# Kernel optimization log

Measured on AMD Instinct MI355X. Metric: run time of the kernel, lower is better.

## Reference

```python
import jax, jax.numpy as jnp
import numpy as np

N_NODES = 100000
N_EDGES = 3200000
N_FEAT = 512
N_GRAPHS = 64
N_EXTRA_LAYERS = 3  # layers 2..4, all 1->1


def setup_inputs() -> dict:
    key = jax.random.key(0)
    ks = jax.random.split(key, 10)
    x = jax.random.normal(ks[0], (N_NODES, N_FEAT), dtype=jnp.float32)
    edge_src = jax.random.randint(ks[1], (N_EDGES,), 0, N_NODES, dtype=jnp.int32)
    edge_dst = jax.random.randint(ks[2], (N_EDGES,), 0, N_NODES, dtype=jnp.int32)
    graph_ids = jnp.sort(jax.random.randint(ks[3], (N_NODES,), 0, N_GRAPHS, dtype=jnp.int32))
    W_neigh0 = jax.random.normal(ks[4], (N_FEAT, 1), dtype=jnp.float32) * 0.05
    W_self0 = jax.random.normal(ks[5], (N_FEAT, 1), dtype=jnp.float32) * 0.05
    b0 = jax.random.normal(ks[6], (1,), dtype=jnp.float32)
    W_neigh_r = jax.random.normal(ks[7], (N_EXTRA_LAYERS, 1, 1), dtype=jnp.float32)
    W_self_r = jax.random.normal(ks[8], (N_EXTRA_LAYERS, 1, 1), dtype=jnp.float32)
    b_r = jax.random.normal(ks[9], (N_EXTRA_LAYERS, 1), dtype=jnp.float32)
    return {"x": x, "edge_src": edge_src, "edge_dst": edge_dst, "graph_ids": graph_ids,
            "W_neigh0": W_neigh0, "W_self0": W_self0, "b0": b0,
            "W_neigh_r": W_neigh_r, "W_self_r": W_self_r, "b_r": b_r}


def _conv_wl(h, edge_src, edge_dst, W_neigh, W_self, b, n_nodes):
    # GraphConv(norm='none'): project first (in >= out here), gather at src, scatter-sum at dst, + bias
    proj = h @ W_neigh                      # [N, out]
    neigh = jax.ops.segment_sum(proj[edge_src], edge_dst, num_segments=n_nodes) + b
    return neigh + h @ W_self               # residual self-loop linear (no bias)


def reference(x, edge_src, edge_dst, graph_ids, W_neigh0, W_self0, b0, W_neigh_r, W_self_r, b_r):
    n = x.shape[0]
    xs = [x]
    h = jax.nn.relu(_conv_wl(x, edge_src, edge_dst, W_neigh0, W_self0, b0, n))
    xs.append(h)
    for i in range(W_neigh_r.shape[0]):
        h = jax.nn.relu(_conv_wl(h, edge_src, edge_dst, W_neigh_r[i], W_self_r[i], b_r[i], n))
        xs.append(h)
    hcat = jnp.concatenate(xs, axis=1)       # [N, F + num_layers] (concat_features=True)
    # dgl.sum_nodes: per-graph sum over the batched graph
    return jax.ops.segment_sum(hcat, graph_ids, num_segments=N_GRAPHS)  # [G, F + L]
```

## Files before the change

kernel.cpp:

```cpp
#include <hip/hip_runtime.h>

#define N_NODES  100000
#define N_EDGES  3200000
#define N_FEAT   512
#define N_GRAPHS 64
#define N_COLS   516
#define NBINS    1563
#define B1       256
#define EPB      (N_EDGES / B1)
#define CHUNK    25
#define NWAVES   (N_NODES / CHUNK)
#define SRC_MASK 0x1FFFF

__global__ __launch_bounds__(1024) void prep_kernel(
    const int* __restrict__ edst, const int* __restrict__ gid,
    int* __restrict__ histG, int* __restrict__ starts, float* __restrict__ outz)
{
    __shared__ int lh[NBINS];
    const int b = blockIdx.x, tid = threadIdx.x;
    const int gtid = b * 1024 + tid;

    if (gtid < N_GRAPHS * N_COLS) outz[gtid] = 0.f;
    if (gtid < N_NODES) {
        const int g = gid[gtid];
        const int gp = gtid ? gid[gtid - 1] : -1;
        for (int q = gp + 1; q <= g; ++q) starts[q] = gtid;
        if (gtid == N_NODES - 1)
            for (int q = g + 1; q <= N_GRAPHS; ++q) starts[q] = N_NODES;
    }
    for (int i = tid; i < NBINS; i += 1024) lh[i] = 0;
    __syncthreads();
    const int e0 = b * EPB;
    for (int e = e0 + tid; e < e0 + EPB; e += 1024)
        atomicAdd(&lh[edst[e] >> 6], 1);
    __syncthreads();
    for (int i = tid; i < NBINS; i += 1024) histG[i * B1 + b] = lh[i];
}

__device__ __forceinline__ void flush_cs(
    int si, int cur_g, const float a[8], int wave, int lane,
    float* __restrict__ pp, int* __restrict__ pt, float* __restrict__ out)
{
    if (si < 2) {
        const int slot = wave * 2 + si;
        if (lane == 0) pt[slot] = cur_g;
        float* d = pp + (size_t)slot * N_FEAT + lane * 8;
        *(float4*)d       = make_float4(a[0], a[1], a[2], a[3]);
        *(float4*)(d + 4) = make_float4(a[4], a[5], a[6], a[7]);
    } else {
        float* o = out + (size_t)cur_g * N_COLS + lane * 8;
        #pragma unroll
        for (int k = 0; k < 8; ++k) atomicAdd(o + k, a[k]);
    }
}

__global__ __launch_bounds__(256) void pass_x_kernel(
    const float* __restrict__ x, const int* __restrict__ gid,
    const float* __restrict__ wn, const float* __restrict__ ws,
    float* __restrict__ p0, float* __restrict__ s0,
    float* __restrict__ neigh, float* __restrict__ out,
    float* __restrict__ pp, int* __restrict__ pt)
{
    const int wave = (blockIdx.x * blockDim.x + threadIdx.x) >> 6;
    const int lane = threadIdx.x & 63;
    const int start = wave * CHUNK, end = start + CHUNK;

    for (int n = start + lane; n < end; n += 64) neigh[n] = 0.f;

    const float4 wna = *(const float4*)(wn + lane * 8);
    const float4 wnb = *(const float4*)(wn + lane * 8 + 4);
    const float4 wsa = *(const float4*)(ws + lane * 8);
    const float4 wsb = *(const float4*)(ws + lane * 8 + 4);

    float a[8] = {0.f, 0.f, 0.f, 0.f, 0.f, 0.f, 0.f, 0.f};
    int cur_g = gid[start];
    const bool uniform = (gid[end - 1] == cur_g);
    int si = 0;

    for (int n = start; n < end; ++n) {
        if (!uniform) {
            const int g = gid[n];
            if (g != cur_g) {
                flush_cs(si, cur_g, a, wave, lane, pp, pt, out);
                ++si;
                #pragma unroll
                for (int k = 0; k < 8; ++k) a[k] = 0.f;
                cur_g = g;
            }
        }
        const float* row = x + (size_t)n * N_FEAT;
        const float4 xa = *(const float4*)(row + lane * 8);
        const float4 xb = *(const float4*)(row + lane * 8 + 4);

        a[0] += xa.x; a[1] += xa.y; a[2] += xa.z; a[3] += xa.w;
        a[4] += xb.x; a[5] += xb.y; a[6] += xb.z; a[7] += xb.w;

        float dn = xa.x*wna.x + xa.y*wna.y + xa.z*wna.z + xa.w*wna.w
                 + xb.x*wnb.x + xb.y*wnb.y + xb.z*wnb.z + xb.w*wnb.w;
        float dv = xa.x*wsa.x + xa.y*wsa.y + xa.z*wsa.z + xa.w*wsa.w
                 + xb.x*wsb.x + xb.y*wsb.y + xb.z*wsb.z + xb.w*wsb.w;
        #pragma unroll
        for (int off = 32; off > 0; off >>= 1) {
            dn += __shfl_down(dn, off);
            dv += __shfl_down(dv, off);
        }
        if (lane == 0) { p0[n] = dn; s0[n] = dv; }
    }
    flush_cs(si, cur_g, a, wave, lane, pp, pt, out);
    ++si;
    if (lane == 0)
        for (int s2 = si; s2 < 2; ++s2) pt[wave * 2 + s2] = -1;
}

__global__ __launch_bounds__(512) void reduce_x_kernel(
    const float* __restrict__ pp, const int* __restrict__ pt,
    const int* __restrict__ starts, float* __restrict__ out)
{
    const int g = blockIdx.x, c = threadIdx.x;
    const int s = starts[g], e = starts[g + 1];
    float acc = 0.f;
    if (e > s) {
        const int w0 = s / CHUNK, w1 = (e - 1) / CHUNK;
        for (int w = w0; w <= w1; ++w) {
            #pragma unroll
            for (int k = 0; k < 2; ++k) {
                const int slot = w * 2 + k;
                if (pt[slot] == g) acc += pp[(size_t)slot * N_FEAT + c];
            }
        }
    }
    out[(size_t)g * N_COLS + c] += acc;
}

__global__ __launch_bounds__(256) void colscan_kernel(
    const int* __restrict__ histG, int* __restrict__ colscanG,
    int* __restrict__ totalG)
{
    __shared__ int sc[256];
    const int bin = blockIdx.x, t = threadIdx.x;
    const int v = histG[bin * B1 + t];
    sc[t] = v;
    __syncthreads();
    for (int off = 1; off < 256; off <<= 1) {
        const int a = (t >= off) ? sc[t - off] : 0;
        __syncthreads();
        sc[t] += a;
        __syncthreads();
    }
    colscanG[bin * B1 + t] = sc[t] - v;
    if (t == 255) totalG[bin] = sc[255];
}

__global__ __launch_bounds__(256) void scan2_kernel(
    const int* __restrict__ totalG, int* __restrict__ binstart)
{
    __shared__ int sc[256];
    const int t = threadIdx.x;
    const int CH = 7;
    int loc[CH];
    int s = 0;
    for (int i = 0; i < CH; ++i) {
        const int bin = t * CH + i;
        const int v = (bin < NBINS) ? totalG[bin] : 0;
        loc[i] = s; s += v;
    }
    const int my = s;
    sc[t] = my;
    __syncthreads();
    for (int off = 1; off < 256; off <<= 1) {
        const int a = (t >= off) ? sc[t - off] : 0;
        __syncthreads();
        sc[t] += a;
        __syncthreads();
    }
    const int texcl = sc[t] - my;
    for (int i = 0; i < CH; ++i) {
        const int bin = t * CH + i;
        if (bin < NBINS) binstart[bin] = texcl + loc[i];
    }
    if (t == 255) binstart[NBINS] = sc[255];
}

__global__ __launch_bounds__(1024) void reorder_kernel(
    const int* __restrict__ esrc, const int* __restrict__ edst,
    const int* __restrict__ binstart, const int* __restrict__ colscanG,
    int* __restrict__ sorted)
{
    __shared__ int offs[NBINS];
    const int b = blockIdx.x, tid = threadIdx.x;
    for (int i = tid; i < NBINS; i += 1024)
        offs[i] = binstart[i] + colscanG[i * B1 + b];
    __syncthreads();
    const int e0 = b * EPB;
    for (int e = e0 + tid; e < e0 + EPB; e += 1024) {
        const int s = esrc[e], d = edst[e];
        const int p = atomicAdd(&offs[d >> 6], 1);
        sorted[p] = s | ((d & 63) << 17);
    }
}

__global__ __launch_bounds__(256) void binned_scatter_kernel(
    const int* __restrict__ sorted, const int* __restrict__ binstart,
    const float* __restrict__ pin, const float* __restrict__ self_in,
    const float* __restrict__ wself_p, const float* __restrict__ bias_p,
    const float* __restrict__ wnext_p,
    float* __restrict__ h_out, float* __restrict__ p_next,
    const int* __restrict__ gid, float* __restrict__ out, int col)
{
    __shared__ float acc[4][64];
    const int b = blockIdx.x, tid = threadIdx.x;
    ((float*)acc)[tid] = 0.f;
    __syncthreads();

    const int st = binstart[b], en = binstart[b + 1];
    const int w = tid >> 6;
    for (int e = st + tid; e < en; e += 256) {
        const int v = sorted[e];
        atomicAdd(&acc[w][v >> 17], pin[v & SRC_MASK]);
    }
    __syncthreads();

    if (tid < 64) {
        const int n = b * 64 + tid;
        const bool valid = (n < N_NODES);
        float h = 0.f;
        int g = 0;
        if (valid) {
            const float nb = acc[0][tid] + acc[1][tid] + acc[2][tid] + acc[3][tid];
            const float sw = wself_p ? *wself_p : 1.0f;
            const float v = nb + *bias_p + sw * self_in[n];
            h = v > 0.f ? v : 0.f;
            h_out[n] = h;
            if (wnext_p) p_next[n] = h * (*wnext_p);
            g = gid[n];
        }
        const int g0 = __shfl(g, 0);
        if (__all(!valid || g == g0)) {
            float s = h;
            #pragma unroll
            for (int off = 32; off > 0; off >>= 1) s += __shfl_down(s, off);
            if (tid == 0) atomicAdd(&out[(size_t)g0 * N_COLS + col], s);
        } else if (valid) {
            atomicAdd(&out[(size_t)g * N_COLS + col], h);
        }
    }
}

extern "C" void kernel_launch(void* const* d_in, const int* in_sizes, int n_in,
                              void* d_out, int out_size, void* d_ws, size_t ws_size,
                              hipStream_t stream)
{
    (void)in_sizes; (void)n_in; (void)out_size; (void)ws_size;

    const float* x    = (const float*)d_in[0];
    const int*   esrc = (const int*)d_in[1];
    const int*   edst = (const int*)d_in[2];
    const int*   gid  = (const int*)d_in[3];
    const float* Wn0  = (const float*)d_in[4];
    const float* Ws0  = (const float*)d_in[5];
    const float* b0p  = (const float*)d_in[6];
    const float* Wnr  = (const float*)d_in[7];
    const float* Wsr  = (const float*)d_in[8];
    const float* brp  = (const float*)d_in[9];
    float* out = (float*)d_out;

    float* pp    = (float*)d_ws;
    float* bufP  = pp + (size_t)NWAVES * 2 * N_FEAT;
    float* bufP2 = bufP  + N_NODES;
    float* bufS  = bufP2 + N_NODES;
    float* bufH  = bufS  + N_NODES;
    int*   pt       = (int*)(bufH + N_NODES);
    int*   starts   = pt + NWAVES * 2;
    int*   binstart = starts + (N_GRAPHS + 1);
    int*   totalG   = binstart + NBINS + 1;
    int*   histG    = totalG + NBINS;
    int*   colscanG = histG + (size_t)NBINS * B1;
    int*   sorted   = colscanG + (size_t)NBINS * B1;

    prep_kernel<<<B1, 1024, 0, stream>>>(edst, gid, histG, starts, out);
    pass_x_kernel<<<NWAVES / 4, 256, 0, stream>>>(
        x, gid, Wn0, Ws0, bufP, bufS, bufP2 ,
        out, pp, pt);
    colscan_kernel<<<NBINS, 256, 0, stream>>>(histG, colscanG, totalG);
    scan2_kernel<<<1, 256, 0, stream>>>(totalG, binstart);
    reorder_kernel<<<B1, 1024, 0, stream>>>(esrc, edst, binstart, colscanG, sorted);
    reduce_x_kernel<<<N_GRAPHS, 512, 0, stream>>>(pp, pt, starts, out);

    binned_scatter_kernel<<<NBINS, 256, 0, stream>>>(
        sorted, binstart, bufP, bufS, nullptr, b0p, Wnr + 0, bufH, bufP2, gid, out, 512);
    binned_scatter_kernel<<<NBINS, 256, 0, stream>>>(
        sorted, binstart, bufP2, bufH, Wsr + 0, brp + 0, Wnr + 1, bufH, bufP, gid, out, 513);
    binned_scatter_kernel<<<NBINS, 256, 0, stream>>>(
        sorted, binstart, bufP, bufH, Wsr + 1, brp + 1, Wnr + 2, bufH, bufP2, gid, out, 514);
    binned_scatter_kernel<<<NBINS, 256, 0, stream>>>(
        sorted, binstart, bufP2, bufH, Wsr + 2, brp + 2, nullptr, bufH, nullptr, gid, out, 515);
}
```

Measured before the change: 508.5 us.

## Fuse scan stages via last-block pattern and merge reorder with graph reduce

Merges the column scan and the global bin scan into one kernel, where the last block to finish (detected with an atomic counter) computes the bin starts. The per-graph reduce is folded into the reorder launch as extra blocks. The x pass now uses nontemporal loads, drops the unused zeroing of the neigh buffer, and uses a smaller node chunk per wave. Together these remove two kernel launches and their tail gaps. The cost is a serialized tail in the last scan block and more partial-sum slots to reduce.

```diff
diff --git a/kernel.cpp b/kernel.cpp
--- a/kernel.cpp
+++ b/kernel.cpp
@@ -8,18 +8,22 @@
 #define NBINS    1563
 #define B1       256
 #define EPB      (N_EDGES / B1)
-#define CHUNK    25
+#define CHUNK    20
 #define NWAVES   (N_NODES / CHUNK)
 #define SRC_MASK 0x1FFFF
 
+typedef float f4v __attribute__((ext_vector_type(4)));
+
 __global__ __launch_bounds__(1024) void prep_kernel(
     const int* __restrict__ edst, const int* __restrict__ gid,
-    int* __restrict__ histG, int* __restrict__ starts, float* __restrict__ outz)
+    int* __restrict__ histG, int* __restrict__ starts,
+    float* __restrict__ outz, int* __restrict__ done)
 {
     __shared__ int lh[NBINS];
     const int b = blockIdx.x, tid = threadIdx.x;
     const int gtid = b * 1024 + tid;
 
+    if (gtid == 0) *done = 0;
     if (gtid < N_GRAPHS * N_COLS) outz[gtid] = 0.f;
     if (gtid < N_NODES) {
         const int g = gid[gtid];
@@ -58,14 +62,11 @@
     const float* __restrict__ x, const int* __restrict__ gid,
     const float* __restrict__ wn, const float* __restrict__ ws,
     float* __restrict__ p0, float* __restrict__ s0,
-    float* __restrict__ neigh, float* __restrict__ out,
-    float* __restrict__ pp, int* __restrict__ pt)
+    float* __restrict__ out, float* __restrict__ pp, int* __restrict__ pt)
 {
     const int wave = (blockIdx.x * blockDim.x + threadIdx.x) >> 6;
     const int lane = threadIdx.x & 63;
     const int start = wave * CHUNK, end = start + CHUNK;
-
-    for (int n = start + lane; n < end; n += 64) neigh[n] = 0.f;
 
     const float4 wna = *(const float4*)(wn + lane * 8);
     const float4 wnb = *(const float4*)(wn + lane * 8 + 4);
@@ -89,8 +90,8 @@
             }
         }
         const float* row = x + (size_t)n * N_FEAT;
-        const float4 xa = *(const float4*)(row + lane * 8);
-        const float4 xb = *(const float4*)(row + lane * 8 + 4);
+        const f4v xa = __builtin_nontemporal_load((const f4v*)(row + lane * 8));
+        const f4v xb = __builtin_nontemporal_load((const f4v*)(row + lane * 8 + 4));
 
         a[0] += xa.x; a[1] += xa.y; a[2] += xa.z; a[3] += xa.w;
         a[4] += xb.x; a[5] += xb.y; a[6] += xb.z; a[7] += xb.w;
@@ -112,31 +113,12 @@
         for (int s2 = si; s2 < 2; ++s2) pt[wave * 2 + s2] = -1;
 }
 
-__global__ __launch_bounds__(512) void reduce_x_kernel(
-    const float* __restrict__ pp, const int* __restrict__ pt,
-    const int* __restrict__ starts, float* __restrict__ out)
-{
-    const int g = blockIdx.x, c = threadIdx.x;
-    const int s = starts[g], e = starts[g + 1];
-    float acc = 0.f;
-    if (e > s) {
-        const int w0 = s / CHUNK, w1 = (e - 1) / CHUNK;
-        for (int w = w0; w <= w1; ++w) {
-            #pragma unroll
-            for (int k = 0; k < 2; ++k) {
-                const int slot = w * 2 + k;
-                if (pt[slot] == g) acc += pp[(size_t)slot * N_FEAT + c];
-            }
-        }
-    }
-    out[(size_t)g * N_COLS + c] += acc;
-}
-
-__global__ __launch_bounds__(256) void colscan_kernel(
+__global__ __launch_bounds__(256) void scan_fused_kernel(
     const int* __restrict__ histG, int* __restrict__ colscanG,
-    int* __restrict__ totalG)
+    int* __restrict__ totalG, int* __restrict__ binstart, int* __restrict__ done)
 {
     __shared__ int sc[256];
+    __shared__ int lastflag;
     const int bin = blockIdx.x, t = threadIdx.x;
     const int v = histG[bin * B1 + t];
     sc[t] = v;
@@ -149,22 +131,23 @@
     }
     colscanG[bin * B1 + t] = sc[t] - v;
     if (t == 255) totalG[bin] = sc[255];
-}
-
-__global__ __launch_bounds__(256) void scan2_kernel(
-    const int* __restrict__ totalG, int* __restrict__ binstart)
-{
-    __shared__ int sc[256];
-    const int t = threadIdx.x;
+
+    __threadfence();
+    if (t == 0) lastflag = (atomicAdd(done, 1) == NBINS - 1);
+    __syncthreads();
+    if (!lastflag) return;
+    __threadfence();
+
     const int CH = 7;
     int loc[CH];
     int s = 0;
     for (int i = 0; i < CH; ++i) {
-        const int bin = t * CH + i;
-        const int v = (bin < NBINS) ? totalG[bin] : 0;
-        loc[i] = s; s += v;
+        const int b2 = t * CH + i;
+        const int vv = (b2 < NBINS) ? totalG[b2] : 0;
+        loc[i] = s; s += vv;
     }
     const int my = s;
+    __syncthreads();
     sc[t] = my;
     __syncthreads();
     for (int off = 1; off < 256; off <<= 1) {
@@ -175,27 +158,47 @@
     }
     const int texcl = sc[t] - my;
     for (int i = 0; i < CH; ++i) {
-        const int bin = t * CH + i;
-        if (bin < NBINS) binstart[bin] = texcl + loc[i];
+        const int b2 = t * CH + i;
+        if (b2 < NBINS) binstart[b2] = texcl + loc[i];
     }
     if (t == 255) binstart[NBINS] = sc[255];
 }
 
-__global__ __launch_bounds__(1024) void reorder_kernel(
+__global__ __launch_bounds__(1024) void reorder_reduce_kernel(
     const int* __restrict__ esrc, const int* __restrict__ edst,
     const int* __restrict__ binstart, const int* __restrict__ colscanG,
-    int* __restrict__ sorted)
-{
-    __shared__ int offs[NBINS];
+    int* __restrict__ sorted,
+    const float* __restrict__ pp, const int* __restrict__ pt,
+    const int* __restrict__ starts, float* __restrict__ out)
+{
     const int b = blockIdx.x, tid = threadIdx.x;
-    for (int i = tid; i < NBINS; i += 1024)
-        offs[i] = binstart[i] + colscanG[i * B1 + b];
-    __syncthreads();
-    const int e0 = b * EPB;
-    for (int e = e0 + tid; e < e0 + EPB; e += 1024) {
-        const int s = esrc[e], d = edst[e];
-        const int p = atomicAdd(&offs[d >> 6], 1);
-        sorted[p] = s | ((d & 63) << 17);
+    if (b < B1) {
+        __shared__ int offs[NBINS];
+        for (int i = tid; i < NBINS; i += 1024)
+            offs[i] = binstart[i] + colscanG[i * B1 + b];
+        __syncthreads();
+        const int e0 = b * EPB;
+        for (int e = e0 + tid; e < e0 + EPB; e += 1024) {
+            const int s = esrc[e], d = edst[e];
+            const int p = atomicAdd(&offs[d >> 6], 1);
+            sorted[p] = s | ((d & 63) << 17);
+        }
+    } else {
+        const int g = (b - B1) * 2 + (tid >> 9);
+        const int c = tid & 511;
+        const int s = starts[g], e = starts[g + 1];
+        float acc = 0.f;
+        if (e > s) {
+            const int w0 = s / CHUNK, w1 = (e - 1) / CHUNK;
+            for (int w = w0; w <= w1; ++w) {
+                #pragma unroll
+                for (int k = 0; k < 2; ++k) {
+                    const int slot = w * 2 + k;
+                    if (pt[slot] == g) acc += pp[(size_t)slot * N_FEAT + c];
+                }
+            }
+        }
+        out[(size_t)g * N_COLS + c] += acc;
     }
 }
 
@@ -273,18 +276,18 @@
     int*   starts   = pt + NWAVES * 2;
     int*   binstart = starts + (N_GRAPHS + 1);
     int*   totalG   = binstart + NBINS + 1;
-    int*   histG    = totalG + NBINS;
+    int*   done     = totalG + NBINS;
+    int*   histG    = done + 1;
     int*   colscanG = histG + (size_t)NBINS * B1;
     int*   sorted   = colscanG + (size_t)NBINS * B1;
 
-    prep_kernel<<<B1, 1024, 0, stream>>>(edst, gid, histG, starts, out);
+    prep_kernel<<<B1, 1024, 0, stream>>>(edst, gid, histG, starts, out, done);
     pass_x_kernel<<<NWAVES / 4, 256, 0, stream>>>(
-        x, gid, Wn0, Ws0, bufP, bufS, bufP2 ,
-        out, pp, pt);
-    colscan_kernel<<<NBINS, 256, 0, stream>>>(histG, colscanG, totalG);
-    scan2_kernel<<<1, 256, 0, stream>>>(totalG, binstart);
-    reorder_kernel<<<B1, 1024, 0, stream>>>(esrc, edst, binstart, colscanG, sorted);
-    reduce_x_kernel<<<N_GRAPHS, 512, 0, stream>>>(pp, pt, starts, out);
+        x, gid, Wn0, Ws0, bufP, bufS, out, pp, pt);
+    scan_fused_kernel<<<NBINS, 256, 0, stream>>>(
+        histG, colscanG, totalG, binstart, done);
+    reorder_reduce_kernel<<<B1 + N_GRAPHS / 2, 1024, 0, stream>>>(
+        esrc, edst, binstart, colscanG, sorted, pp, pt, starts, out);
 
     binned_scatter_kernel<<<NBINS, 256, 0, stream>>>(
         sorted, binstart, bufP, bufS, nullptr, b0p, Wnr + 0, bufH, bufP2, gid, out, 512);
```

After: 614.3 us. 20.8% more time.
